# Kernel optimization log

Measured on AMD Instinct MI355X. Metric: run time of the kernel, lower is better.

## Reference

```python
import jax, jax.numpy as jnp
import numpy as np

B, S, D, H, DFF = 4, 2048, 1024, 16, 4096
DK = D // H
EPS = 1e-6


def setup_inputs() -> dict:
    key = jax.random.key(0)
    ks = jax.random.split(key, 20)
    p = lambda k, shape: jax.random.normal(k, shape, dtype=jnp.float32) * 0.02
    inp = {
        "x": jax.random.normal(ks[0], (B, S, D), dtype=jnp.float32),
        "src_mask": jax.random.randint(ks[1], (B, 1, 1, S), 0, 2, dtype=jnp.int32),
        "Wq": p(ks[2], (D, D)), "bq": jnp.zeros((D,), jnp.float32),
        "Wk": p(ks[3], (D, D)), "bk": jnp.zeros((D,), jnp.float32),
        "Wv": p(ks[4], (D, D)), "bv": jnp.zeros((D,), jnp.float32),
        "Wo": p(ks[5], (D, D)), "bo": jnp.zeros((D,), jnp.float32),
        "W1": p(ks[6], (D, DFF)), "b1": jnp.zeros((DFF,), jnp.float32),
        "W2": p(ks[7], (DFF, D)), "b2": jnp.zeros((D,), jnp.float32),
        "ln1_a": jnp.ones((D,), jnp.float32), "ln1_b": jnp.zeros((D,), jnp.float32),
        "ln2_a": jnp.ones((D,), jnp.float32), "ln2_b": jnp.zeros((D,), jnp.float32),
    }
    return inp


def _layer_norm(x, a, b):
    # Faithful to source: unbiased std (torch default) and divide by (std + eps)
    mean = jnp.mean(x, axis=-1, keepdims=True)
    std = jnp.std(x, axis=-1, ddof=1, keepdims=True)
    return a * (x - mean) / (std + EPS) + b


def reference(x, src_mask, Wq, bq, Wk, bk, Wv, bv, Wo, bo, W1, b1, W2, b2,
              ln1_a, ln1_b, ln2_a, ln2_b):
    # Multi-head self-attention (dropout = identity, eval mode)
    q = (x @ Wq + bq).reshape(B, S, H, DK)
    k = (x @ Wk + bk).reshape(B, S, H, DK)
    v = (x @ Wv + bv).reshape(B, S, H, DK)
    scores = jnp.einsum("bqhd,bkhd->bhqk", q, k) / jnp.sqrt(jnp.float32(DK))
    scores = jnp.where(src_mask == 0, jnp.float32(-1e9), scores)
    attn = jax.nn.softmax(scores, axis=-1)
    ctx = jnp.einsum("bhqk,bkhd->bqhd", attn, v).reshape(B, S, D)
    attn_out = ctx @ Wo + bo

    x = _layer_norm(x + attn_out, ln1_a, ln1_b)

    # FeedForward: linear -> relu -> (dropout=identity) -> linear
    ff = jax.nn.relu(x @ W1 + b1) @ W2 + b2
    x = _layer_norm(x + ff, ln2_a, ln2_b)
    return x
```

## Files before the change

kernel.cpp:

```cpp
#include <hip/hip_runtime.h>

#define Bn 4
#define Sn 2048
#define Dn 1024
#define Hn 16
#define DKn 64
#define DFFn 4096
#define Mn (Bn * Sn)
#define QKVS 3072

typedef __bf16 bf16;
typedef __attribute__((ext_vector_type(8))) __bf16 bf16x8;
typedef __attribute__((ext_vector_type(4))) __bf16 bf16x4;
typedef __attribute__((ext_vector_type(8))) unsigned short u16x8;
typedef __attribute__((ext_vector_type(4))) float f32x4;
typedef __attribute__((ext_vector_type(16))) float f32x16;

#define LOG2E_DIV8 0.18033688011112042f

__device__ __forceinline__ float exp2fast(float x) {
  return __builtin_amdgcn_exp2f(x);
}

__device__ __forceinline__ void glds16(const bf16* g, bf16* l) {
  __builtin_amdgcn_global_load_lds((const __attribute__((address_space(1))) void*)g,
                                   (__attribute__((address_space(3))) void*)l, 16, 0, 0);
}

__device__ __forceinline__ unsigned int pkbf16(float a, float b) {
  union { __bf16 h[2]; unsigned int u; } x;
  x.h[0] = (__bf16)a; x.h[1] = (__bf16)b;
  return x.u;
}

__global__ __launch_bounds__(256) void k_cvt_bf16(const float* __restrict__ in,
                                                  bf16* __restrict__ out) {
  size_t i = ((size_t)blockIdx.x * 256 + threadIdx.x) * 8;
  f32x4 a = *(const f32x4*)(in + i);
  f32x4 b = *(const f32x4*)(in + i + 4);
  bf16x8 o;
#pragma unroll
  for (int j = 0; j < 4; ++j) { o[j] = (bf16)a[j]; o[j + 4] = (bf16)b[j]; }
  *(bf16x8*)(out + i) = o;
}

__global__ __launch_bounds__(256) void k_transpose_bf16(const float* __restrict__ in,
                                                        bf16* __restrict__ out,
                                                        int K, int N, float scale) {
  __shared__ float tile[32][33];
  int n0 = blockIdx.x * 32, k0 = blockIdx.y * 32;
  int tx = threadIdx.x, ty = threadIdx.y;
#pragma unroll
  for (int j = ty; j < 32; j += 8)
    tile[j][tx] = in[(size_t)(k0 + j) * N + n0 + tx];
  __syncthreads();
#pragma unroll
  for (int j = ty; j < 32; j += 8)
    out[(size_t)(n0 + j) * K + k0 + tx] = (bf16)(tile[tx][j] * scale);
}

__global__ __launch_bounds__(256) void k_bias3(const float* __restrict__ bq,
                                               const float* __restrict__ bk,
                                               const float* __restrict__ bv,
                                               float* __restrict__ o) {
  int i = blockIdx.x * 256 + threadIdx.x;
  float v = (i < 1024) ? bq[i] * LOG2E_DIV8
          : (i < 2048) ? bk[i - 1024] : bv[i - 2048];
  o[i] = v;
}

__global__ __launch_bounds__(256) void k_vt(const bf16* __restrict__ v,
                                            bf16* __restrict__ vT, int vs) {
  __shared__ bf16 T[64][72];
  const int t = threadIdx.x;
  const int s0 = blockIdx.x * 64;
  const int bh = blockIdx.y, b = bh >> 4, h = bh & 15;
#pragma unroll
  for (int it = 0; it < 2; ++it) {
    int r = (t >> 3) + it * 32;
    int c = t & 7;
    u16x8 val = *(const u16x8*)(v + (size_t)(b * Sn + s0 + r) * vs + h * 64 + c * 8);
    *(u16x8*)&T[r][c * 8] = val;
  }
  __syncthreads();
#pragma unroll
  for (int it = 0; it < 2; ++it) {
    int d = (t >> 3) + it * 32;
    int cs = t & 7;
    bf16x8 o;
#pragma unroll
    for (int j = 0; j < 8; ++j) o[j] = T[cs * 8 + j][d];
    *(bf16x8*)(vT + ((size_t)bh * 64 + d) * Sn + s0 + cs * 8) = o;
  }
}

template <int NFRAG, int DO_RELU>
__global__ __launch_bounds__(512, 2) void k_gemm256(const bf16* __restrict__ A,
                                                    const bf16* __restrict__ BT,
                                                    const float* __restrict__ bias,
                                                    bf16* __restrict__ C,
                                                    int Ndim, int Kdim) {
  __shared__ __align__(128) bf16 Asm[2][256 * 64];
  __shared__ __align__(128) bf16 Bsm[2][NFRAG * 64 * 64];
  const int tid = threadIdx.x;
  const int wid = tid >> 6, lane = tid & 63;
  const int l15 = lane & 15, l4 = lane >> 4;
  const int wm = wid >> 2, wn = wid & 3;

  const int gx = gridDim.x;
  int lin = blockIdx.y * gx + blockIdx.x;
  const int nwg = gx * gridDim.y;
  lin = (lin & 7) * (nwg >> 3) + (lin >> 3);
  const int m0 = (lin / gx) * 256;
  const int n0 = (lin % gx) * (NFRAG * 64);

  f32x4 acc[8][NFRAG];
#pragma unroll
  for (int mf = 0; mf < 8; ++mf)
#pragma unroll
    for (int nf = 0; nf < NFRAG; ++nf) acc[mf][nf] = f32x4{0.f, 0.f, 0.f, 0.f};

  const int lr = lane >> 3, lc = lane & 7;
  const int NT = Kdim >> 6;

#define STAGE(buf, t)                                                              \
  {                                                                                \
    _Pragma("unroll") for (int it = 0; it < 4; ++it) {                             \
      int r = it * 64 + wid * 8 + lr;                                              \
      int ch = lc ^ (r & 7);                                                       \
      glds16(A + (size_t)(m0 + r) * Kdim + (size_t)(t) * 64 + ch * 8,              \
             &Asm[buf][(it * 64 + wid * 8) * 64]);                                 \
    }                                                                              \
    _Pragma("unroll") for (int it = 0; it < NFRAG; ++it) {                         \
      int r = it * 64 + wid * 8 + lr;                                              \
      int ch = lc ^ (r & 7);                                                       \
      glds16(BT + (size_t)(n0 + r) * Kdim + (size_t)(t) * 64 + ch * 8,             \
             &Bsm[buf][(it * 64 + wid * 8) * 64]);                                 \
    }                                                                              \
  }

  int p = 0;
  STAGE(0, 0);
  for (int t = 0; t < NT; ++t) {
    if (t + 1 < NT) {
      STAGE(p ^ 1, t + 1);
      if constexpr (NFRAG == 4) asm volatile("s_waitcnt vmcnt(8)" ::: "memory");
      else                      asm volatile("s_waitcnt vmcnt(6)" ::: "memory");
    } else {
      asm volatile("s_waitcnt vmcnt(0)" ::: "memory");
    }
    __builtin_amdgcn_sched_barrier(0);
    __builtin_amdgcn_s_barrier();

    bf16x8 bfrag[NFRAG][2];
#pragma unroll
    for (int nf = 0; nf < NFRAG; ++nf)
#pragma unroll
      for (int kk = 0; kk < 2; ++kk) {
        int r = wn * (NFRAG * 16) + nf * 16 + l15;
        int ch = (kk * 4 + l4) ^ (r & 7);
        bfrag[nf][kk] = *(const bf16x8*)&Bsm[p][r * 64 + ch * 8];
      }
#pragma unroll
    for (int half = 0; half < 2; ++half) {
      bf16x8 afr[4][2];
#pragma unroll
      for (int mf4 = 0; mf4 < 4; ++mf4)
#pragma unroll
        for (int kk = 0; kk < 2; ++kk) {
          int r = wm * 128 + half * 64 + mf4 * 16 + l15;
          int ch = (kk * 4 + l4) ^ (r & 7);
          afr[mf4][kk] = *(const bf16x8*)&Asm[p][r * 64 + ch * 8];
        }
      __builtin_amdgcn_s_setprio(1);
#pragma unroll
      for (int mf4 = 0; mf4 < 4; ++mf4)
#pragma unroll
        for (int nf = 0; nf < NFRAG; ++nf)
#pragma unroll
          for (int kk = 0; kk < 2; ++kk)
            acc[half * 4 + mf4][nf] = __builtin_amdgcn_mfma_f32_16x16x32_bf16(
                afr[mf4][kk], bfrag[nf][kk], acc[half * 4 + mf4][nf], 0, 0, 0);
      __builtin_amdgcn_s_setprio(0);
    }
    __builtin_amdgcn_s_barrier();
    p ^= 1;
  }
#undef STAGE

#pragma unroll
  for (int mf = 0; mf < 8; ++mf)
#pragma unroll
    for (int nf = 0; nf < NFRAG; ++nf) {
      int c = n0 + wn * (NFRAG * 16) + nf * 16 + l15;
      float bv = bias[c];
      int r0 = m0 + wm * 128 + mf * 16 + l4 * 4;
#pragma unroll
      for (int r = 0; r < 4; ++r) {
        float val = acc[mf][nf][r] + bv;
        if (DO_RELU) val = fmaxf(val, 0.f);
        C[(size_t)(r0 + r) * Ndim + c] = (bf16)val;
      }
    }
}

__global__ __launch_bounds__(256) void k_attn(const bf16* __restrict__ q,
                                              const bf16* __restrict__ k,
                                              const bf16* __restrict__ vT,
                                              const int* __restrict__ mask,
                                              bf16* __restrict__ ctx, int qs) {
  __shared__ __align__(128) bf16 Kt[2][64 * 64];
  __shared__ __align__(128) bf16 Vt[2][64 * 64];
  __shared__ float Mb[Sn];
  const int tid = threadIdx.x, wid = tid >> 6, lane = tid & 63;
  const int q31 = lane & 31, hi = lane >> 5;

  int lin = blockIdx.y * gridDim.x + blockIdx.x;
  lin = (lin & 7) * 128 + (lin >> 3);
  const int qblk = lin & 15, bh = lin >> 4;
  const int b = bh >> 4, h = bh & 15;
  const int q0 = qblk * 128 + wid * 32;

  for (int i = tid; i < Sn; i += 256)
    Mb[i] = mask[b * Sn + i] ? 0.f : -1.44269504e9f;

  bf16x8 qf[4];
#pragma unroll
  for (int t = 0; t < 4; ++t)
    qf[t] = *(const bf16x8*)(q + (size_t)(b * Sn + q0 + q31) * qs + h * 64 +
                             t * 16 + hi * 8);

  f32x16 o[2];
  o[0] = {}; o[1] = {};
  float mr = -INFINITY, lr = 0.f;

  const int lrow = lane >> 3;
  const int lch0 = lane & 7;

  for (int kb = 0; kb < Sn / 64; ++kb) {
    const int cur = kb & 1;
    if (kb == 0) {
#pragma unroll
      for (int s = 0; s < 2; ++s) {
        int row = (wid + 4 * s) * 8 + lrow;
        int ch = lch0 ^ (lrow ^ ((wid + 4 * s) & 3));
        glds16(k + (size_t)(b * Sn + row) * qs + h * 64 + ch * 8,
               &Kt[0][(wid + 4 * s) * 512]);
        glds16(vT + ((size_t)bh * 64 + row) * Sn + ch * 8,
               &Vt[0][(wid + 4 * s) * 512]);
      }
      __syncthreads();
    }
    if (kb + 1 < Sn / 64) {
#pragma unroll
      for (int s = 0; s < 2; ++s) {
        int row = (wid + 4 * s) * 8 + lrow;
        int ch = lch0 ^ (lrow ^ ((wid + 4 * s) & 3));
        glds16(k + (size_t)(b * Sn + (kb + 1) * 64 + row) * qs + h * 64 + ch * 8,
               &Kt[cur ^ 1][(wid + 4 * s) * 512]);
        glds16(vT + ((size_t)bh * 64 + row) * Sn + (kb + 1) * 64 + ch * 8,
               &Vt[cur ^ 1][(wid + 4 * s) * 512]);
      }
    }

    f32x16 sc[2];
#pragma unroll
    for (int kf = 0; kf < 2; ++kf)
#pragma unroll
      for (int rg = 0; rg < 4; ++rg) {
        f32x4 mb4 = *(const f32x4*)&Mb[kb * 64 + kf * 32 + rg * 8 + 4 * hi];
#pragma unroll
        for (int j = 0; j < 4; ++j) sc[kf][rg * 4 + j] = mb4[j];
      }
#pragma unroll
    for (int t = 0; t < 4; ++t) {
#pragma unroll
      for (int kf = 0; kf < 2; ++kf) {
        int row = kf * 32 + q31;
        int ch = (t * 2 + hi) ^ ((row & 7) ^ ((row >> 3) & 3));
        bf16x8 kfr = *(const bf16x8*)&Kt[cur][row * 64 + ch * 8];
        sc[kf] = __builtin_amdgcn_mfma_f32_32x32x16_bf16(kfr, qf[t], sc[kf], 0, 0, 0);
      }
    }

    float rmax = fmaxf(sc[0][0], sc[0][1]);
#pragma unroll
    for (int i = 2; i < 16; i += 2)
      rmax = fmaxf(fmaxf(rmax, sc[0][i]), sc[0][i + 1]);
#pragma unroll
    for (int i = 0; i < 16; i += 2)
      rmax = fmaxf(fmaxf(rmax, sc[1][i]), sc[1][i + 1]);
    rmax = fmaxf(rmax, __shfl_xor(rmax, 32));

    if (!__all(rmax <= mr + 8.f)) {
      float mnew = fmaxf(mr, rmax);
      float psc = exp2fast(mr - mnew);
      mr = mnew;
      lr *= psc;
#pragma unroll
      for (int af = 0; af < 2; ++af)
#pragma unroll
        for (int i = 0; i < 16; ++i) o[af][i] *= psc;
    }

    float psum = 0.f;
#pragma unroll
    for (int kf = 0; kf < 2; ++kf)
#pragma unroll
      for (int i = 0; i < 16; ++i) {
        float p = exp2fast(sc[kf][i] - mr);
        sc[kf][i] = p;
        psum += p;
      }
    psum += __shfl_xor(psum, 32);
    lr += psum;

#pragma unroll
    for (int ks = 0; ks < 4; ++ks) {
      const int kf = ks >> 1, R = (ks & 1) * 8;
      unsigned int a0 = pkbf16(sc[kf][R + 0], sc[kf][R + 1]);
      unsigned int a1 = pkbf16(sc[kf][R + 2], sc[kf][R + 3]);
      unsigned int b0 = pkbf16(sc[kf][R + 4], sc[kf][R + 5]);
      unsigned int b1 = pkbf16(sc[kf][R + 6], sc[kf][R + 7]);
      unsigned int sxa0 = __shfl_xor(a0, 32), sxa1 = __shfl_xor(a1, 32);
      unsigned int sxb0 = __shfl_xor(b0, 32), sxb1 = __shfl_xor(b1, 32);
      union { unsigned int w[4]; bf16x8 v; } pfu;
      pfu.w[0] = hi ? sxb0 : a0;
      pfu.w[1] = hi ? sxb1 : a1;
      pfu.w[2] = hi ? b0 : sxa0;
      pfu.w[3] = hi ? b1 : sxa1;
#pragma unroll
      for (int af = 0; af < 2; ++af) {
        int row = af * 32 + q31;
        int ch = (ks * 2 + hi) ^ ((row & 7) ^ ((row >> 3) & 3));
        bf16x8 vfr = *(const bf16x8*)&Vt[cur][row * 64 + ch * 8];
        o[af] = __builtin_amdgcn_mfma_f32_32x32x16_bf16(vfr, pfu.v, o[af], 0, 0, 0);
      }
    }
    __syncthreads();
  }

  float inv = 1.f / lr;
  const size_t cbase = (size_t)(b * Sn + q0 + q31) * Dn + h * 64;
#pragma unroll
  for (int af = 0; af < 2; ++af)
#pragma unroll
    for (int rg = 0; rg < 4; ++rg) {
      bf16x4 ov;
#pragma unroll
      for (int j = 0; j < 4; ++j) ov[j] = (bf16)(o[af][rg * 4 + j] * inv);
      *(bf16x4*)(ctx + cbase + af * 32 + rg * 8 + 4 * hi) = ov;
    }
}

template <int XF32, int OUTF32>
__global__ __launch_bounds__(256) void k_ln(const void* __restrict__ xp,
                                            const bf16* __restrict__ res,
                                            const float* __restrict__ gamma,
                                            const float* __restrict__ beta,
                                            void* __restrict__ yout) {
  const int row = blockIdx.x, t = threadIdx.x;
  const size_t base = (size_t)row * Dn + t * 4;
  f32x4 a;
  if constexpr (XF32) {
    a = *(const f32x4*)((const float*)xp + base);
  } else {
    bf16x4 x4 = *(const bf16x4*)((const bf16*)xp + base);
#pragma unroll
    for (int j = 0; j < 4; ++j) a[j] = (float)x4[j];
  }
  bf16x4 rb = *(const bf16x4*)(res + base);
  f32x4 vv;
#pragma unroll
  for (int j = 0; j < 4; ++j) vv[j] = a[j] + (float)rb[j];

  float s = vv[0] + vv[1] + vv[2] + vv[3];
#pragma unroll
  for (int off = 32; off; off >>= 1) s += __shfl_xor(s, off);
  __shared__ float red1[4], red2[4];
  if ((t & 63) == 0) red1[t >> 6] = s;
  __syncthreads();
  float mean = (red1[0] + red1[1] + red1[2] + red1[3]) * (1.f / 1024.f);

  float d[4], s2 = 0.f;
#pragma unroll
  for (int j = 0; j < 4; ++j) { d[j] = vv[j] - mean; s2 += d[j] * d[j]; }
#pragma unroll
  for (int off = 32; off; off >>= 1) s2 += __shfl_xor(s2, off);
  if ((t & 63) == 0) red2[t >> 6] = s2;
  __syncthreads();
  float var = (red2[0] + red2[1] + red2[2] + red2[3]) * (1.f / 1023.f);
  float inv = 1.f / (sqrtf(var) + 1e-6f);

  f32x4 g = *(const f32x4*)(gamma + t * 4);
  f32x4 bt = *(const f32x4*)(beta + t * 4);
#pragma unroll
  for (int j = 0; j < 4; ++j) d[j] = g[j] * d[j] * inv + bt[j];
  if constexpr (OUTF32) {
    f32x4 outv = {d[0], d[1], d[2], d[3]};
    *(f32x4*)((float*)yout + base) = outv;
  } else {
    bf16x4 outb;
#pragma unroll
    for (int j = 0; j < 4; ++j) outb[j] = (bf16)d[j];
    *(bf16x4*)((bf16*)yout + base) = outb;
  }
}

extern "C" void kernel_launch(void* const* d_in, const int* in_sizes, int n_in,
                              void* d_out, int out_size, void* d_ws, size_t ws_size,
                              hipStream_t stream) {
  const float* x   = (const float*)d_in[0];
  const int*   msk = (const int*)d_in[1];
  const float* Wq  = (const float*)d_in[2];
  const float* bq  = (const float*)d_in[3];
  const float* Wk  = (const float*)d_in[4];
  const float* bk  = (const float*)d_in[5];
  const float* Wv  = (const float*)d_in[6];
  const float* bv  = (const float*)d_in[7];
  const float* Wo  = (const float*)d_in[8];
  const float* bo  = (const float*)d_in[9];
  const float* W1  = (const float*)d_in[10];
  const float* b1  = (const float*)d_in[11];
  const float* W2  = (const float*)d_in[12];
  const float* b2  = (const float*)d_in[13];
  const float* g1  = (const float*)d_in[14];
  const float* be1 = (const float*)d_in[15];
  const float* g2  = (const float*)d_in[16];
  const float* be2 = (const float*)d_in[17];
  float* out = (float*)d_out;

  char* w = (char*)d_ws;
  size_t off = 0;
  auto alloc = [&](size_t bytes) { void* p = w + off; off += (bytes + 255) & ~(size_t)255; return p; };
  bf16* xb    = (bf16*)alloc((size_t)Mn * Dn * 2);
  bf16* wqkvT = (bf16*)alloc((size_t)QKVS * Dn * 2);
  bf16* woT   = (bf16*)alloc((size_t)Dn * Dn * 2);
  bf16* w1T   = (bf16*)alloc((size_t)Dn * DFFn * 2);
  bf16* w2T   = (bf16*)alloc((size_t)DFFn * Dn * 2);
  float* bqkv = (float*)alloc((size_t)QKVS * 4);
  bf16* qkv   = (bf16*)alloc((size_t)Mn * QKVS * 2);
  bf16* ctx   = (bf16*)alloc((size_t)Mn * Dn * 2);
  bf16* attnb = (bf16*)alloc((size_t)Mn * Dn * 2);
  bf16* yb    = (bf16*)alloc((size_t)Mn * Dn * 2);
  (void)ws_size; (void)in_sizes; (void)n_in; (void)out_size;
  bf16* vT = xb;
  bf16* hh = qkv;
  bf16* ff = xb;

  k_cvt_bf16<<<(Mn * Dn) / 2048, 256, 0, stream>>>(x, xb);
  dim3 tb(32, 8);
  k_transpose_bf16<<<dim3(32, 32), tb, 0, stream>>>(Wq, wqkvT, Dn, Dn, LOG2E_DIV8);
  k_transpose_bf16<<<dim3(32, 32), tb, 0, stream>>>(Wk, wqkvT + (size_t)1024 * Dn, Dn, Dn, 1.f);
  k_transpose_bf16<<<dim3(32, 32), tb, 0, stream>>>(Wv, wqkvT + (size_t)2048 * Dn, Dn, Dn, 1.f);
  k_transpose_bf16<<<dim3(32, 32), tb, 0, stream>>>(Wo, woT, Dn, Dn, 1.f);
  k_transpose_bf16<<<dim3(128, 32), tb, 0, stream>>>(W1, w1T, Dn, DFFn, 1.f);
  k_transpose_bf16<<<dim3(32, 128), tb, 0, stream>>>(W2, w2T, DFFn, Dn, 1.f);
  k_bias3<<<QKVS / 256, 256, 0, stream>>>(bq, bk, bv, bqkv);

  k_gemm256<4, 0><<<dim3(QKVS / 256, Mn / 256), 512, 0, stream>>>(xb, wqkvT, bqkv, qkv, QKVS, Dn);

  k_vt<<<dim3(Sn / 64, Bn * Hn), 256, 0, stream>>>(qkv + 2048, vT, QKVS);
  k_attn<<<dim3(Sn / 128, Bn * Hn), 256, 0, stream>>>(qkv, qkv + 1024, vT, msk, ctx, QKVS);

  k_gemm256<2, 0><<<dim3(Dn / 128, Mn / 256), 512, 0, stream>>>(ctx, woT, bo, attnb, Dn, Dn);

  k_ln<1, 0><<<Mn, 256, 0, stream>>>(x, attnb, g1, be1, yb);

  k_gemm256<4, 1><<<dim3(DFFn / 256, Mn / 256), 512, 0, stream>>>(yb, w1T, b1, hh, DFFn, Dn);

  k_gemm256<2, 0><<<dim3(Dn / 128, Mn / 256), 512, 0, stream>>>(hh, w2T, b2, ff, Dn, DFFn);

  k_ln<0, 1><<<Mn, 256, 0, stream>>>(yb, ff, g2, be2, out);
}
```

Before: 457.3 us.

## Fuse weight-prep kernels and double attention block to 8 waves per K/V tile

All six weight transposes and the QKV bias packing are merged into one launch, replacing seven kernel launches with one. The attention kernel now uses 512 threads (8 waves) covering 256 queries per block, so each K/V tile loaded into LDS serves twice as many queries and each wave issues one staging load per buffer instead of two. This halves redundant K/V global traffic and mask staging per query, at the cost of fewer blocks (512), which may affect occupancy and tail balance.

```diff
diff --git a/kernel.cpp b/kernel.cpp
--- a/kernel.cpp
+++ b/kernel.cpp
@@ -44,12 +44,52 @@
   *(bf16x8*)(out + i) = o;
 }
 
-__global__ __launch_bounds__(256) void k_transpose_bf16(const float* __restrict__ in,
-                                                        bf16* __restrict__ out,
-                                                        int K, int N, float scale) {
+__global__ __launch_bounds__(256) void k_prep(const float* __restrict__ Wq,
+                                              const float* __restrict__ Wk,
+                                              const float* __restrict__ Wv,
+                                              const float* __restrict__ Wo,
+                                              const float* __restrict__ W1,
+                                              const float* __restrict__ W2,
+                                              const float* __restrict__ bq,
+                                              const float* __restrict__ bk,
+                                              const float* __restrict__ bv,
+                                              bf16* __restrict__ wqkvT,
+                                              bf16* __restrict__ woT,
+                                              bf16* __restrict__ w1T,
+                                              bf16* __restrict__ w2T,
+                                              float* __restrict__ bqkv) {
   __shared__ float tile[32][33];
-  int n0 = blockIdx.x * 32, k0 = blockIdx.y * 32;
-  int tx = threadIdx.x, ty = threadIdx.y;
+  const int id = blockIdx.x, t = threadIdx.x;
+  if (id >= 12288) {
+    int j = (id - 12288) * 256 + t;
+    float v = (j < 1024) ? bq[j] * LOG2E_DIV8
+            : (j < 2048) ? bk[j - 1024] : bv[j - 2048];
+    bqkv[j] = v;
+    return;
+  }
+  const float* in;
+  bf16* out;
+  int K, N, bx, by;
+  float scale = 1.f;
+  if (id < 4096) {
+    int z = id >> 10, local = id & 1023;
+    bx = local & 31; by = local >> 5;
+    K = Dn; N = Dn;
+    if (z == 0)      { in = Wq; out = wqkvT; scale = LOG2E_DIV8; }
+    else if (z == 1) { in = Wk; out = wqkvT + (size_t)1024 * Dn; }
+    else if (z == 2) { in = Wv; out = wqkvT + (size_t)2048 * Dn; }
+    else             { in = Wo; out = woT; }
+  } else if (id < 8192) {
+    int local = id - 4096;
+    bx = local & 127; by = local >> 7;
+    K = Dn; N = DFFn; in = W1; out = w1T;
+  } else {
+    int local = id - 8192;
+    bx = local & 31; by = local >> 5;
+    K = DFFn; N = Dn; in = W2; out = w2T;
+  }
+  const int n0 = bx * 32, k0 = by * 32;
+  const int tx = t & 31, ty = t >> 5;
 #pragma unroll
   for (int j = ty; j < 32; j += 8)
     tile[j][tx] = in[(size_t)(k0 + j) * N + n0 + tx];
@@ -57,16 +97,6 @@
 #pragma unroll
   for (int j = ty; j < 32; j += 8)
     out[(size_t)(n0 + j) * K + k0 + tx] = (bf16)(tile[tx][j] * scale);
-}
-
-__global__ __launch_bounds__(256) void k_bias3(const float* __restrict__ bq,
-                                               const float* __restrict__ bk,
-                                               const float* __restrict__ bv,
-                                               float* __restrict__ o) {
-  int i = blockIdx.x * 256 + threadIdx.x;
-  float v = (i < 1024) ? bq[i] * LOG2E_DIV8
-          : (i < 2048) ? bk[i - 1024] : bv[i - 2048];
-  o[i] = v;
 }
 
 __global__ __launch_bounds__(256) void k_vt(const bf16* __restrict__ v,
@@ -204,7 +234,7 @@
     }
 }
 
-__global__ __launch_bounds__(256) void k_attn(const bf16* __restrict__ q,
+__global__ __launch_bounds__(512) void k_attn(const bf16* __restrict__ q,
                                               const bf16* __restrict__ k,
                                               const bf16* __restrict__ vT,
                                               const int* __restrict__ mask,
@@ -216,12 +246,12 @@
   const int q31 = lane & 31, hi = lane >> 5;
 
   int lin = blockIdx.y * gridDim.x + blockIdx.x;
-  lin = (lin & 7) * 128 + (lin >> 3);
-  const int qblk = lin & 15, bh = lin >> 4;
+  lin = (lin & 7) * 64 + (lin >> 3);
+  const int qblk = lin & 7, bh = lin >> 3;
   const int b = bh >> 4, h = bh & 15;
-  const int q0 = qblk * 128 + wid * 32;
-
-  for (int i = tid; i < Sn; i += 256)
+  const int q0 = qblk * 256 + wid * 32;
+
+  for (int i = tid; i < Sn; i += 512)
     Mb[i] = mask[b * Sn + i] ? 0.f : -1.44269504e9f;
 
   bf16x8 qf[4];
@@ -236,31 +266,22 @@
 
   const int lrow = lane >> 3;
   const int lch0 = lane & 7;
+  const int sch = lch0 ^ (lrow ^ (wid & 3));
 
   for (int kb = 0; kb < Sn / 64; ++kb) {
     const int cur = kb & 1;
     if (kb == 0) {
-#pragma unroll
-      for (int s = 0; s < 2; ++s) {
-        int row = (wid + 4 * s) * 8 + lrow;
-        int ch = lch0 ^ (lrow ^ ((wid + 4 * s) & 3));
-        glds16(k + (size_t)(b * Sn + row) * qs + h * 64 + ch * 8,
-               &Kt[0][(wid + 4 * s) * 512]);
-        glds16(vT + ((size_t)bh * 64 + row) * Sn + ch * 8,
-               &Vt[0][(wid + 4 * s) * 512]);
-      }
+      int row = wid * 8 + lrow;
+      glds16(k + (size_t)(b * Sn + row) * qs + h * 64 + sch * 8, &Kt[0][wid * 512]);
+      glds16(vT + ((size_t)bh * 64 + row) * Sn + sch * 8, &Vt[0][wid * 512]);
       __syncthreads();
     }
     if (kb + 1 < Sn / 64) {
-#pragma unroll
-      for (int s = 0; s < 2; ++s) {
-        int row = (wid + 4 * s) * 8 + lrow;
-        int ch = lch0 ^ (lrow ^ ((wid + 4 * s) & 3));
-        glds16(k + (size_t)(b * Sn + (kb + 1) * 64 + row) * qs + h * 64 + ch * 8,
-               &Kt[cur ^ 1][(wid + 4 * s) * 512]);
-        glds16(vT + ((size_t)bh * 64 + row) * Sn + (kb + 1) * 64 + ch * 8,
-               &Vt[cur ^ 1][(wid + 4 * s) * 512]);
-      }
+      int row = wid * 8 + lrow;
+      glds16(k + (size_t)(b * Sn + (kb + 1) * 64 + row) * qs + h * 64 + sch * 8,
+             &Kt[cur ^ 1][wid * 512]);
+      glds16(vT + ((size_t)bh * 64 + row) * Sn + (kb + 1) * 64 + sch * 8,
+             &Vt[cur ^ 1][wid * 512]);
     }
 
     f32x16 sc[2];
@@ -449,19 +470,13 @@
   bf16* ff = xb;
 
   k_cvt_bf16<<<(Mn * Dn) / 2048, 256, 0, stream>>>(x, xb);
-  dim3 tb(32, 8);
-  k_transpose_bf16<<<dim3(32, 32), tb, 0, stream>>>(Wq, wqkvT, Dn, Dn, LOG2E_DIV8);
-  k_transpose_bf16<<<dim3(32, 32), tb, 0, stream>>>(Wk, wqkvT + (size_t)1024 * Dn, Dn, Dn, 1.f);
-  k_transpose_bf16<<<dim3(32, 32), tb, 0, stream>>>(Wv, wqkvT + (size_t)2048 * Dn, Dn, Dn, 1.f);
-  k_transpose_bf16<<<dim3(32, 32), tb, 0, stream>>>(Wo, woT, Dn, Dn, 1.f);
-  k_transpose_bf16<<<dim3(128, 32), tb, 0, stream>>>(W1, w1T, Dn, DFFn, 1.f);
-  k_transpose_bf16<<<dim3(32, 128), tb, 0, stream>>>(W2, w2T, DFFn, Dn, 1.f);
-  k_bias3<<<QKVS / 256, 256, 0, stream>>>(bq, bk, bv, bqkv);
+  k_prep<<<12300, 256, 0, stream>>>(Wq, Wk, Wv, Wo, W1, W2, bq, bk, bv,
+                                    wqkvT, woT, w1T, w2T, bqkv);
 
   k_gemm256<4, 0><<<dim3(QKVS / 256, Mn / 256), 512, 0, stream>>>(xb, wqkvT, bqkv, qkv, QKVS, Dn);
 
   k_vt<<<dim3(Sn / 64, Bn * Hn), 256, 0, stream>>>(qkv + 2048, vT, QKVS);
-  k_attn<<<dim3(Sn / 128, Bn * Hn), 256, 0, stream>>>(qkv, qkv + 1024, vT, msk, ctx, QKVS);
+  k_attn<<<dim3(Sn / 256, Bn * Hn), 512, 0, stream>>>(qkv, qkv + 1024, vT, msk, ctx, QKVS);
 
   k_gemm256<2, 0><<<dim3(Dn / 128, Mn / 256), 512, 0, stream>>>(ctx, woT, bo, attnb, Dn, Dn);
 
```

Result: faster. 414.0 us (-9.5%).
